# Performance work log

Measured on AMD Instinct MI355X. Metric: run time of the kernel, lower is better.

## Reference

```python
import math
import jax, jax.numpy as jnp
import numpy as np

WINDOW = 7
N_HEAD = 12
DIM_HEAD = 32
DIM = 384
SHIFT = True
BATCH, H, W = 16, 56, 56


def _create_mask(ws, d, upper_lower, left_right):
    m = np.zeros((ws * ws, ws * ws), dtype=np.float32)
    if upper_lower:
        m[-d * ws:, :-d * ws] = 1
        m[:-d * ws, -d * ws:] = 1
    if left_right:
        m = m.reshape(ws, ws, ws, ws)
        m[:, -d:, :, :-d] = float('-inf')
        m[:, :-d, :, -d:] = float('-inf')
        m = m.reshape(ws * ws, ws * ws)
    return m

# Faithful to torch: `> 0` comparison (note lr_mask ends up all-False since -inf > 0 is False)
_D = WINDOW // 2
UL_MASK = jnp.asarray(_create_mask(WINDOW, _D, True, False) > 0)
LR_MASK = jnp.asarray(_create_mask(WINDOW, _D, False, True) > 0)


def _pos_index():
    idx = np.stack(np.meshgrid(np.arange(WINDOW), np.arange(WINDOW), indexing='ij'), -1).reshape(-1, 2)
    dist = idx[None, :, :] - idx[:, None, :] + (WINDOW - 1)  # (49,49,2)
    return jnp.asarray(dist[..., 0] * (2 * WINDOW - 1) + dist[..., 1])  # (49,49)

POS = _pos_index()


def setup_inputs() -> dict:
    key = jax.random.key(0)
    k1, k2, k3, k4, k5 = jax.random.split(key, 5)
    scale = 1.0 / math.sqrt(DIM)
    return {
        'x': jax.random.normal(k1, (BATCH, H, W, DIM), dtype=jnp.float32),
        'w_qkv': jax.random.normal(k2, (3 * N_HEAD * DIM_HEAD, DIM), dtype=jnp.float32) * scale,
        'w_out': jax.random.normal(k3, (DIM, N_HEAD * DIM_HEAD), dtype=jnp.float32) * scale,
        'b_out': jax.random.normal(k4, (DIM,), dtype=jnp.float32) * 0.01,
        'rel_pos_table': jax.random.normal(k5, ((2 * WINDOW - 1) ** 2, N_HEAD), dtype=jnp.float32) * 0.02,
    }


def reference(x, w_qkv, w_out, b_out, rel_pos_table):
    b, height, width, _ = x.shape
    hs, ws = height // WINDOW, width // WINDOW
    roll = -(WINDOW // 2)
    if SHIFT:
        x = jnp.roll(x, (roll, roll), axis=(1, 2))
    qkv = x @ w_qkv.T  # (b,H,W,3*nh*dh)
    q, k, v = jnp.split(qkv, 3, axis=-1)

    def resh(t):
        t = t.reshape(b, hs, WINDOW, ws, WINDOW, N_HEAD, DIM_HEAD)
        return t.transpose(0, 5, 1, 3, 2, 4, 6).reshape(b, N_HEAD, hs * ws, WINDOW * WINDOW, DIM_HEAD)

    q, k, v = resh(q), resh(k), resh(v)
    score = jnp.einsum('bhwqd,bhwkd->bhwqk', q, k) / math.sqrt(DIM_HEAD)
    rel = rel_pos_table[POS]  # (49,49,nh)
    score = score + rel.transpose(2, 0, 1)[None, :, None]  # broadcast over windows
    if SHIFT:
        score = score.at[:, :, -ws:].set(jnp.where(UL_MASK, -jnp.inf, score[:, :, -ws:]))
        score = score.at[:, :, ws - 1::ws].set(jnp.where(LR_MASK, -jnp.inf, score[:, :, ws - 1::ws]))
    attn = jax.nn.softmax(score, axis=-1)
    out = jnp.einsum('bhwqk,bhwkd->bhwqd', attn, v)
    out = out.reshape(b, N_HEAD, hs, ws, WINDOW, WINDOW, DIM_HEAD)
    out = out.transpose(0, 2, 4, 3, 5, 1, 6).reshape(b, height, width, N_HEAD * DIM_HEAD)
    out = out @ w_out.T + b_out
    if SHIFT:
        out = jnp.roll(out, (-roll, -roll), axis=(1, 2))
    return out
```

## Files before the change

### kernel.cpp

```cpp
#include <hip/hip_runtime.h>

typedef unsigned short u16;
typedef short bf16x8 __attribute__((ext_vector_type(8)));
typedef float f32x4 __attribute__((ext_vector_type(4)));

#define MFMA16(a,b,c) __builtin_amdgcn_mfma_f32_16x16x32_bf16((a),(b),(c),0,0,0)
#define NEGHUGE (-1.0e30f)

__device__ __forceinline__ u16 f2b(float f){
  union { float f; unsigned int i; } v; v.f = f;
  unsigned int r = v.i + 0x7FFFu + ((v.i>>16)&1u);
  return (u16)(r>>16);
}

union BfPack { u16 h[8]; bf16x8 v; uint4 u; };

__device__ __forceinline__ uint4 pack8u(const float* __restrict__ p){
  float4 a = *(const float4*)p;
  float4 b = *(const float4*)(p + 4);
  BfPack r;
  r.h[0]=f2b(a.x); r.h[1]=f2b(a.y); r.h[2]=f2b(a.z); r.h[3]=f2b(a.w);
  r.h[4]=f2b(b.x); r.h[5]=f2b(b.y); r.h[6]=f2b(b.z); r.h[7]=f2b(b.w);
  return r.u;
}

__device__ __forceinline__ void gld_lds16(const u16* g, u16* l){
  __builtin_amdgcn_global_load_lds(
      (const __attribute__((address_space(1))) unsigned int*)g,
      (__attribute__((address_space(3))) unsigned int*)l, 16, 0, 0);
}

__global__ __launch_bounds__(256) void k_convert(
    const float* __restrict__ x, const float* __restrict__ wqkv,
    const float* __restrict__ wout,
    u16* __restrict__ xb, u16* __restrict__ wqkvp, u16* __restrict__ woutp)
{
  int idx = (int)blockIdx.x * 256 + threadIdx.x;
  if (idx < 2408448) {
    *(uint4*)(xb + (size_t)idx*8) = pack8u(x + (size_t)idx*8);
  } else if (idx < 2463744) {
    int u = idx - 2408448;
    int nf = u / 768, rem = u - nf*768, k = rem >> 6, l = rem & 63;
    const float* src = wqkv + (size_t)(nf*16 + (l & 15))*384 + k*32 + (l >> 4)*8;
    *(uint4*)(wqkvp + (size_t)u*8) = pack8u(src);
  } else {
    int u = idx - 2463744;
    int nf = u / 768, rem = u - nf*768, k = rem >> 6, l = rem & 63;
    const float* src = wout + (size_t)(nf*16 + (l & 15))*384 + k*32 + (l >> 4)*8;
    *(uint4*)(woutp + (size_t)u*8) = pack8u(src);
  }
}

__global__ __launch_bounds__(768, 3) void k_fused(
    const u16* __restrict__ xb, const u16* __restrict__ wqkvp,
    const u16* __restrict__ woutp, const float* __restrict__ bout,
    const float* __restrict__ relt, float* __restrict__ out)
{
  __shared__ u16 R1[64*384];
  __shared__ u16 QKs[12][49*64];
  __shared__ float relb[12][169];

  const int tid = threadIdx.x;
  const int wv = tid >> 6, lane = tid & 63, quad = lane >> 4, l16 = lane & 15;
  const int blk = (int)blockIdx.x;
  const int b = blk >> 6, win = blk & 63, hb = win >> 3, wb = win & 7;

  u16* qk = &QKs[wv][0];
  u16* At = R1;
  u16* vt = R1 + wv*2048;

  for (int i = lane; i < 169; i += 64) relb[wv][i] = relt[i*12 + wv];

  #pragma unroll
  for (int i = 0; i < 4; ++i) {
    const int u = i*768 + tid;
    if (u < 2352) {
      const int r = u / 48, c = u - r*48;
      const int cl = c ^ (r & 7);
      const int py = r / 7, px = r - py*7;
      int hh = hb*7 + py + 3; if (hh >= 56) hh -= 56;
      int ww = wb*7 + px + 3; if (ww >= 56) ww -= 56;
      gld_lds16(xb + (size_t)((b*56 + hh)*56 + ww)*384 + cl*8,
                At + (size_t)(i*768 + (tid & ~63))*8);
    }
  }
  __syncthreads();

  f32x4 accA[4][4];
  #pragma unroll
  for (int mi = 0; mi < 4; ++mi)
    #pragma unroll
    for (int f = 0; f < 4; ++f) accA[mi][f] = f32x4{0.f,0.f,0.f,0.f};

  for (int k = 0; k < 12; ++k) {
    bf16x8 a[4], bb[4];
    #pragma unroll
    for (int mi = 0; mi < 4; ++mi) {
      int row = mi*16 + l16; if (row > 48) row = 48;
      a[mi] = *(const bf16x8*)(At + row*384 + (((k*4 + quad) ^ (row & 7)) << 3));
    }
    #pragma unroll
    for (int f = 0; f < 4; ++f) {
      const int nf = (f >> 1)*24 + wv*2 + (f & 1);
      bb[f] = *(const bf16x8*)(wqkvp + ((size_t)(nf*12 + k)*64 + lane)*8);
    }
    #pragma unroll
    for (int mi = 0; mi < 4; ++mi)
      #pragma unroll
      for (int f = 0; f < 4; ++f)
        accA[mi][f] = MFMA16(a[mi], bb[f], accA[mi][f]);
  }

  #pragma unroll
  for (int mi = 0; mi < 4; ++mi)
    #pragma unroll
    for (int r = 0; r < 4; ++r) {
      const int pos = mi*16 + quad*4 + r;
      if (pos < 49) {
        const int swq = (pos >> 1) & 7;
        #pragma unroll
        for (int f = 0; f < 4; ++f) {
          const int c = (f >> 1)*4 + (f & 1)*2 + (l16 >> 3);
          qk[pos*64 + ((c ^ swq) << 3) + (l16 & 7)] = f2b(accA[mi][f][r]);
        }
      }
    }

  f32x4 accB[4][2];
  #pragma unroll
  for (int mi = 0; mi < 4; ++mi)
    #pragma unroll
    for (int f = 0; f < 2; ++f) accB[mi][f] = f32x4{0.f,0.f,0.f,0.f};

  for (int k = 0; k < 12; ++k) {
    bf16x8 a[4], bb[2];
    #pragma unroll
    for (int mi = 0; mi < 4; ++mi) {
      int row = mi*16 + l16; if (row > 48) row = 48;
      a[mi] = *(const bf16x8*)(At + row*384 + (((k*4 + quad) ^ (row & 7)) << 3));
    }
    #pragma unroll
    for (int f = 0; f < 2; ++f) {
      const int nf = 48 + wv*2 + f;
      bb[f] = *(const bf16x8*)(wqkvp + ((size_t)(nf*12 + k)*64 + lane)*8);
    }
    #pragma unroll
    for (int mi = 0; mi < 4; ++mi)
      #pragma unroll
      for (int f = 0; f < 2; ++f)
        accB[mi][f] = MFMA16(a[mi], bb[f], accB[mi][f]);
  }
  __syncthreads();

  #pragma unroll
  for (int i = 0; i < 4; ++i)
    *(uint4*)(vt + (i*64 + lane)*8) = uint4{0,0,0,0};
  #pragma unroll
  for (int mi = 0; mi < 4; ++mi)
    #pragma unroll
    for (int r = 0; r < 4; ++r) {
      const int pos = mi*16 + quad*4 + r;
      if (pos < 49) {
        #pragma unroll
        for (int f = 0; f < 2; ++f) {
          const int d = f*16 + l16;
          vt[d*64 + (((pos >> 3) ^ (d & 7)) << 3) + (pos & 7)] = f2b(accB[mi][f][r]);
        }
      }
    }

  bf16x8 aq[4], bk[4];
  #pragma unroll
  for (int mt = 0; mt < 4; ++mt) {
    int p2 = mt*16 + l16; if (p2 > 48) p2 = 48;
    aq[mt] = *(const bf16x8*)(qk + p2*64 + ((quad ^ ((p2 >> 1) & 7)) << 3));
  }
  #pragma unroll
  for (int n = 0; n < 4; ++n) {
    int kp = n*16 + l16; if (kp > 48) kp = 48;
    bk[n] = *(const bf16x8*)(qk + kp*64 + (((4 + quad) ^ ((kp >> 1) & 7)) << 3));
  }
  f32x4 sc[4][4];
  #pragma unroll
  for (int mt = 0; mt < 4; ++mt)
    #pragma unroll
    for (int n = 0; n < 4; ++n) {
      f32x4 z = {0.f,0.f,0.f,0.f};
      sc[mt][n] = MFMA16(aq[mt], bk[n], z);
    }

  #pragma unroll
  for (int mt = 0; mt < 4; ++mt)
    #pragma unroll
    for (int r = 0; r < 4; ++r) {
      const int q = mt*16 + quad*4 + r;
      const int qy = q / 7, qx = q - qy*7;
      #pragma unroll
      for (int n = 0; n < 4; ++n) {
        const int key = n*16 + l16;
        float s = sc[mt][n][r] * 0.17677669529663687f;
        if (key < 49 && q < 49) {
          const int ky = key / 7, kx = key - ky*7;
          s += relb[wv][(ky - qy + 6)*13 + (kx - qx + 6)];
          if (hb == 7 && ((qy >= 4) != (ky >= 4))) s = NEGHUGE;
        } else {
          s = NEGHUGE;
        }
        sc[mt][n][r] = s;
      }
      float sum = 0.f;
      #pragma unroll
      for (int n = 0; n < 4; ++n) {
        float p = exp2f((sc[mt][n][r] - 8.0f) * 1.4426950408889634f);
        sc[mt][n][r] = p; sum += p;
      }
      sum += __shfl_xor(sum, 1);
      sum += __shfl_xor(sum, 2);
      sum += __shfl_xor(sum, 4);
      sum += __shfl_xor(sum, 8);
      const float rinv = 1.0f / sum;
      if (q < 49) {
        const int swq = (q >> 1) & 7;
        #pragma unroll
        for (int n = 0; n < 4; ++n)
          qk[q*64 + (((n*2 + (l16 >> 3)) ^ swq) << 3) + (l16 & 7)] =
              f2b(sc[mt][n][r] * rinv);
      }
    }

  #pragma unroll
  for (int mt = 0; mt < 4; ++mt) {
    int rp = mt*16 + l16; if (rp > 48) rp = 48;
    const int swp = (rp >> 1) & 7;
    const bf16x8 ap0 = *(const bf16x8*)(qk + rp*64 + ((quad ^ swp) << 3));
    const bf16x8 ap1 = *(const bf16x8*)(qk + rp*64 + (((4+quad) ^ swp) << 3));
    #pragma unroll
    for (int n2 = 0; n2 < 2; ++n2) {
      const int d = n2*16 + l16;
      const bf16x8 bv0 = *(const bf16x8*)(vt + d*64 + ((quad ^ (d & 7)) << 3));
      const bf16x8 bv1 = *(const bf16x8*)(vt + d*64 + (((4+quad) ^ (d & 7)) << 3));
      f32x4 o = {0.f,0.f,0.f,0.f};
      o = MFMA16(ap0, bv0, o);
      o = MFMA16(ap1, bv1, o);
      #pragma unroll
      for (int r = 0; r < 4; ++r) {
        const int q = mt*16 + quad*4 + r;
        if (q < 49) qk[q*40 + n2*16 + l16] = f2b(o[r]);
      }
    }
  }
  __syncthreads();

  f32x4 pacc[4][2];
  #pragma unroll
  for (int mi = 0; mi < 4; ++mi)
    #pragma unroll
    for (int j = 0; j < 2; ++j) pacc[mi][j] = f32x4{0.f,0.f,0.f,0.f};

  for (int k = 0; k < 12; ++k) {
    bf16x8 a[4], bb[2];
    #pragma unroll
    for (int mi = 0; mi < 4; ++mi) {
      int row = mi*16 + l16; if (row > 48) row = 48;
      a[mi] = *(const bf16x8*)(&QKs[k][row*40 + quad*8]);
    }
    #pragma unroll
    for (int j = 0; j < 2; ++j) {
      const int nf = wv*2 + j;
      bb[j] = *(const bf16x8*)(woutp + ((size_t)(nf*12 + k)*64 + lane)*8);
    }
    #pragma unroll
    for (int mi = 0; mi < 4; ++mi)
      #pragma unroll
      for (int j = 0; j < 2; ++j)
        pacc[mi][j] = MFMA16(a[mi], bb[j], pacc[mi][j]);
  }

  float bias[2];
  #pragma unroll
  for (int j = 0; j < 2; ++j) bias[j] = bout[wv*32 + j*16 + l16];

  #pragma unroll
  for (int mi = 0; mi < 4; ++mi)
    #pragma unroll
    for (int r = 0; r < 4; ++r) {
      const int q = mi*16 + quad*4 + r;
      if (q < 49) {
        const int py = q / 7, px = q - py*7;
        int hh = hb*7 + py + 3; if (hh >= 56) hh -= 56;
        int ww = wb*7 + px + 3; if (ww >= 56) ww -= 56;
        float* dst = out + (size_t)((b*56 + hh)*56 + ww)*384 + wv*32;
        #pragma unroll
        for (int j = 0; j < 2; ++j)
          dst[j*16 + l16] = pacc[mi][j][r] + bias[j];
      }
    }
}

extern "C" void kernel_launch(void* const* d_in, const int* in_sizes, int n_in,
                              void* d_out, int out_size, void* d_ws, size_t ws_size,
                              hipStream_t stream) {
  const float* x    = (const float*)d_in[0];
  const float* wqkv = (const float*)d_in[1];
  const float* wout = (const float*)d_in[2];
  const float* bout = (const float*)d_in[3];
  const float* relt = (const float*)d_in[4];

  char* ws = (char*)d_ws;
  u16* xb    = (u16*)(ws);
  u16* wqkvp = (u16*)(ws + 38535168);
  u16* woutp = (u16*)(ws + 39419904);
  float* outp = (float*)d_out;

  k_convert<<<9696, 256, 0, stream>>>(x, wqkv, wout, xb, wqkvp, woutp);
  k_fused<<<1024, 768, 0, stream>>>(xb, wqkvp, woutp, bout, relt, outp);
}
```

Baseline: 287.0 us.

## Fuse x fp32-to-bf16 conversion into fused kernel load and restructure attention loop

Drops the separate pass that converted the whole input x to bf16 in workspace. The fused kernel now reads fp32 x directly, packs it to bf16 in registers and stores it into swizzled LDS, so the bf16 copy of x is no longer written to and read back from global memory. The attention part is also restructured into a per-row-tile loop (unroll 1) that computes scores, softmax and PV per tile, with K and V fragments hoisted, to lower register pressure. The cost is twice the global read bytes per block and a synchronous load path in place of the async global_load_lds.

```diff
diff --git a/kernel.cpp b/kernel.cpp
--- a/kernel.cpp
+++ b/kernel.cpp
@@ -24,35 +24,21 @@
   return r.u;
 }
 
-__device__ __forceinline__ void gld_lds16(const u16* g, u16* l){
-  __builtin_amdgcn_global_load_lds(
-      (const __attribute__((address_space(1))) unsigned int*)g,
-      (__attribute__((address_space(3))) unsigned int*)l, 16, 0, 0);
-}
-
-__global__ __launch_bounds__(256) void k_convert(
-    const float* __restrict__ x, const float* __restrict__ wqkv,
-    const float* __restrict__ wout,
-    u16* __restrict__ xb, u16* __restrict__ wqkvp, u16* __restrict__ woutp)
+__global__ __launch_bounds__(256) void k_convert_w(
+    const float* __restrict__ wqkv, const float* __restrict__ wout,
+    u16* __restrict__ wqkvp, u16* __restrict__ woutp)
 {
   int idx = (int)blockIdx.x * 256 + threadIdx.x;
-  if (idx < 2408448) {
-    *(uint4*)(xb + (size_t)idx*8) = pack8u(x + (size_t)idx*8);
-  } else if (idx < 2463744) {
-    int u = idx - 2408448;
-    int nf = u / 768, rem = u - nf*768, k = rem >> 6, l = rem & 63;
-    const float* src = wqkv + (size_t)(nf*16 + (l & 15))*384 + k*32 + (l >> 4)*8;
-    *(uint4*)(wqkvp + (size_t)u*8) = pack8u(src);
-  } else {
-    int u = idx - 2463744;
-    int nf = u / 768, rem = u - nf*768, k = rem >> 6, l = rem & 63;
-    const float* src = wout + (size_t)(nf*16 + (l & 15))*384 + k*32 + (l >> 4)*8;
-    *(uint4*)(woutp + (size_t)u*8) = pack8u(src);
-  }
+  const float* W; u16* dst; int u;
+  if (idx < 55296) { W = wqkv; dst = wqkvp; u = idx; }
+  else             { W = wout; dst = woutp; u = idx - 55296; }
+  int nf = u / 768, rem = u - nf*768, k = rem >> 6, l = rem & 63;
+  const float* src = W + (size_t)(nf*16 + (l & 15))*384 + k*32 + (l >> 4)*8;
+  *(uint4*)(dst + (size_t)u*8) = pack8u(src);
 }
 
 __global__ __launch_bounds__(768, 3) void k_fused(
-    const u16* __restrict__ xb, const u16* __restrict__ wqkvp,
+    const float* __restrict__ x, const u16* __restrict__ wqkvp,
     const u16* __restrict__ woutp, const float* __restrict__ bout,
     const float* __restrict__ relt, float* __restrict__ out)
 {
@@ -76,12 +62,11 @@
     const int u = i*768 + tid;
     if (u < 2352) {
       const int r = u / 48, c = u - r*48;
-      const int cl = c ^ (r & 7);
       const int py = r / 7, px = r - py*7;
       int hh = hb*7 + py + 3; if (hh >= 56) hh -= 56;
       int ww = wb*7 + px + 3; if (ww >= 56) ww -= 56;
-      gld_lds16(xb + (size_t)((b*56 + hh)*56 + ww)*384 + cl*8,
-                At + (size_t)(i*768 + (tid & ~63))*8);
+      uint4 v = pack8u(x + (size_t)((b*56 + hh)*56 + ww)*384 + c*8);
+      *(uint4*)(At + (size_t)(r*48 + (c ^ (r & 7)))*8) = v;
     }
   }
   __syncthreads();
@@ -169,28 +154,31 @@
       }
     }
 
-  bf16x8 aq[4], bk[4];
-  #pragma unroll
+  bf16x8 bkf[4];
+  #pragma unroll
+  for (int n = 0; n < 4; ++n) {
+    int kp = n*16 + l16; if (kp > 48) kp = 48;
+    bkf[n] = *(const bf16x8*)(qk + kp*64 + (((4 + quad) ^ ((kp >> 1) & 7)) << 3));
+  }
+  bf16x8 bv0[2], bv1[2];
+  #pragma unroll
+  for (int n2 = 0; n2 < 2; ++n2) {
+    const int d = n2*16 + l16;
+    bv0[n2] = *(const bf16x8*)(vt + d*64 + ((quad ^ (d & 7)) << 3));
+    bv1[n2] = *(const bf16x8*)(vt + d*64 + (((4+quad) ^ (d & 7)) << 3));
+  }
+
+  #pragma unroll 1
   for (int mt = 0; mt < 4; ++mt) {
     int p2 = mt*16 + l16; if (p2 > 48) p2 = 48;
-    aq[mt] = *(const bf16x8*)(qk + p2*64 + ((quad ^ ((p2 >> 1) & 7)) << 3));
-  }
-  #pragma unroll
-  for (int n = 0; n < 4; ++n) {
-    int kp = n*16 + l16; if (kp > 48) kp = 48;
-    bk[n] = *(const bf16x8*)(qk + kp*64 + (((4 + quad) ^ ((kp >> 1) & 7)) << 3));
-  }
-  f32x4 sc[4][4];
-  #pragma unroll
-  for (int mt = 0; mt < 4; ++mt)
+    const bf16x8 aq = *(const bf16x8*)(qk + p2*64 + ((quad ^ ((p2 >> 1) & 7)) << 3));
+    f32x4 sc[4];
     #pragma unroll
     for (int n = 0; n < 4; ++n) {
       f32x4 z = {0.f,0.f,0.f,0.f};
-      sc[mt][n] = MFMA16(aq[mt], bk[n], z);
-    }
-
-  #pragma unroll
-  for (int mt = 0; mt < 4; ++mt)
+      sc[n] = MFMA16(aq, bkf[n], z);
+    }
+
     #pragma unroll
     for (int r = 0; r < 4; ++r) {
       const int q = mt*16 + quad*4 + r;
@@ -198,7 +186,7 @@
       #pragma unroll
       for (int n = 0; n < 4; ++n) {
         const int key = n*16 + l16;
-        float s = sc[mt][n][r] * 0.17677669529663687f;
+        float s = sc[n][r] * 0.17677669529663687f;
         if (key < 49 && q < 49) {
           const int ky = key / 7, kx = key - ky*7;
           s += relb[wv][(ky - qy + 6)*13 + (kx - qx + 6)];
@@ -206,13 +194,13 @@
         } else {
           s = NEGHUGE;
         }
-        sc[mt][n][r] = s;
+        sc[n][r] = s;
       }
       float sum = 0.f;
       #pragma unroll
       for (int n = 0; n < 4; ++n) {
-        float p = exp2f((sc[mt][n][r] - 8.0f) * 1.4426950408889634f);
-        sc[mt][n][r] = p; sum += p;
+        float p = exp2f((sc[n][r] - 8.0f) * 1.4426950408889634f);
+        sc[n][r] = p; sum += p;
       }
       sum += __shfl_xor(sum, 1);
       sum += __shfl_xor(sum, 2);
@@ -224,28 +212,25 @@
         #pragma unroll
         for (int n = 0; n < 4; ++n)
           qk[q*64 + (((n*2 + (l16 >> 3)) ^ swq) << 3) + (l16 & 7)] =
-              f2b(sc[mt][n][r] * rinv);
-      }
-    }
-
-  #pragma unroll
-  for (int mt = 0; mt < 4; ++mt) {
-    int rp = mt*16 + l16; if (rp > 48) rp = 48;
-    const int swp = (rp >> 1) & 7;
-    const bf16x8 ap0 = *(const bf16x8*)(qk + rp*64 + ((quad ^ swp) << 3));
-    const bf16x8 ap1 = *(const bf16x8*)(qk + rp*64 + (((4+quad) ^ swp) << 3));
-    #pragma unroll
-    for (int n2 = 0; n2 < 2; ++n2) {
-      const int d = n2*16 + l16;
-      const bf16x8 bv0 = *(const bf16x8*)(vt + d*64 + ((quad ^ (d & 7)) << 3));
-      const bf16x8 bv1 = *(const bf16x8*)(vt + d*64 + (((4+quad) ^ (d & 7)) << 3));
-      f32x4 o = {0.f,0.f,0.f,0.f};
-      o = MFMA16(ap0, bv0, o);
-      o = MFMA16(ap1, bv1, o);
-      #pragma unroll
-      for (int r = 0; r < 4; ++r) {
-        const int q = mt*16 + quad*4 + r;
-        if (q < 49) qk[q*40 + n2*16 + l16] = f2b(o[r]);
+              f2b(sc[n][r] * rinv);
+      }
+    }
+
+    {
+      int rp = mt*16 + l16; if (rp > 48) rp = 48;
+      const int swp = (rp >> 1) & 7;
+      const bf16x8 ap0 = *(const bf16x8*)(qk + rp*64 + ((quad ^ swp) << 3));
+      const bf16x8 ap1 = *(const bf16x8*)(qk + rp*64 + (((4+quad) ^ swp) << 3));
+      #pragma unroll
+      for (int n2 = 0; n2 < 2; ++n2) {
+        f32x4 o = {0.f,0.f,0.f,0.f};
+        o = MFMA16(ap0, bv0[n2], o);
+        o = MFMA16(ap1, bv1[n2], o);
+        #pragma unroll
+        for (int r = 0; r < 4; ++r) {
+          const int q = mt*16 + quad*4 + r;
+          if (q < 49) qk[q*40 + n2*16 + l16] = f2b(o[r]);
+        }
       }
     }
   }
@@ -307,11 +292,10 @@
   const float* relt = (const float*)d_in[4];
 
   char* ws = (char*)d_ws;
-  u16* xb    = (u16*)(ws);
-  u16* wqkvp = (u16*)(ws + 38535168);
-  u16* woutp = (u16*)(ws + 39419904);
+  u16* wqkvp = (u16*)(ws);
+  u16* woutp = (u16*)(ws + 884736);
   float* outp = (float*)d_out;
 
-  k_convert<<<9696, 256, 0, stream>>>(x, wqkv, wout, xb, wqkvp, woutp);
-  k_fused<<<1024, 768, 0, stream>>>(xb, wqkvp, woutp, bout, relt, outp);
-}
+  k_convert_w<<<288, 256, 0, stream>>>(wqkv, wout, wqkvp, woutp);
+  k_fused<<<1024, 768, 0, stream>>>(x, wqkvp, woutp, bout, relt, outp);
+}
```

Result: no change. 286.7 us (-0.1%).
